# Kernel optimization log

Hardware: AMD Instinct MI355X
Metric: run time of the kernel (lower is better)

## Reference

```python
import jax, jax.numpy as jnp
import numpy as np
import math

LAMB = 0.2
N_ITERS = 3
HALF_PLUS_HALF_LOG2PI = 0.5 + 0.5 * math.log(2.0 * math.pi)  # 1/2 + log(2*pi)/2
SQRT_2PI = math.sqrt(2.0 * math.pi)


def _safe_div(num, den):
    # tf.math.divide_no_nan: 0 where denominator is 0
    den_ok = jnp.where(den == 0, 1.0, den)
    return jnp.where(den == 0, 0.0, num / den_ok)


def _m_step(act_in, R, V, bias_a, bias_b):
    # act_in: [B,ci], R: [B or 1,ci,co], V: [B,ci,co,q,s]
    odds = act_in[:, :, None] * R                                        # [B,ci,co]
    r = _safe_div(odds, jnp.sum(odds, axis=1, keepdims=True))[:, :, :, None, None]
    mu = jnp.sum(r * V, axis=1, keepdims=True)                           # [B,1,co,q,s]
    sigma = jnp.sqrt(jnp.sum(r * (V - mu) ** 2, axis=1, keepdims=True))  # [B,1,co,q,s]
    cost = jnp.sum(r * jnp.log(sigma) + HALF_PLUS_HALF_LOG2PI, axis=1)   # [B,co,q,s]
    logits = LAMB * (bias_a
                     - bias_b * jnp.sum(r, axis=(1, 3, 4))
                     - jnp.sum(cost, axis=(2, 3)))                       # [B,co]
    act_out = jax.nn.softmax(logits, axis=-1)
    return act_out, jnp.sum(mu, axis=1), sigma                           # mu -> [B,co,q,s]


def _e_step(act_out, V, mu, sigma):
    # Normal(mu, sigma).prob(V); mu broadcast over capsules_in axis
    d = V - mu[:, None]                                                  # [B,ci,co,q,s]
    prob = jnp.exp(-0.5 * d * d / (sigma * sigma)) / (sigma * SQRT_2PI)
    raw_R = act_out[:, None, :, None, None] * prob                       # [B,ci,co,q,s]
    # tf.linalg.norm(ord=1, axis=None) = global sum of |raw_R| over the whole tensor
    normed = _safe_div(raw_R, jnp.sum(jnp.abs(raw_R)))
    return jnp.sum(normed, axis=(3, 4))                                  # [B,ci,co]


def setup_inputs() -> dict:
    key = jax.random.key(0)
    k1, k2, k3, k4, k5 = jax.random.split(key, 5)
    B, CI, CO, P, S = 16, 512, 128, 8, 8
    act = jax.random.uniform(k1, (B, CI), dtype=jnp.float32)
    pose = jax.random.normal(k2, (B, CI, P, P), dtype=jnp.float32)
    transitions = 0.05 * jax.random.normal(k3, (CI, CO, P, S), dtype=jnp.float32)
    bias_a = 0.05 * jax.random.normal(k4, (CO,), dtype=jnp.float32)
    bias_b = 0.05 * jax.random.normal(k5, (CO,), dtype=jnp.float32)
    return {"act": act, "pose": pose, "transitions": transitions,
            "bias_a": bias_a, "bias_b": bias_b}


def reference(act, pose, transitions, bias_a, bias_b):
    CI = act.shape[1]
    CO = transitions.shape[1]
    posed = jnp.swapaxes(pose, -1, -2)                 # transPOSE=True
    # votes: pose[:, :, None, :, :] @ transitions  -> [B,ci,co,q,s]
    V = jnp.einsum('biqp,iops->bioqs', posed, transitions)
    R = jnp.full((1, CI, CO), 1.0 / CO, dtype=V.dtype)
    act_out, mu, sigma = _m_step(act, R, V, bias_a, bias_b)
    for _ in range(N_ITERS - 1):
        R = _e_step(act_out, V, mu, sigma)
        act_out, mu, sigma = _m_step(act, R, V, bias_a, bias_b)
    return act_out, mu
```

## Files before the change

### kernel.cpp

```cpp
#include <hip/hip_runtime.h>
#include <hip/hip_bf16.h>

#define B_    16
#define CI_   512
#define CO_   128
#define QS    64
#define NWAVE 16
#define IPW   (CI_ / NWAVE)

static constexpr float LAMB = 0.2f;
static constexpr float NEG_HALF_LOG2E = -0.72134752044448170368f;

template <int CTRL>
__device__ __forceinline__ float dpp_add(float v) {
    int x = __builtin_bit_cast(int, v);
    int y = __builtin_amdgcn_update_dpp(x, x, CTRL, 0xF, 0xF, false);
    return v + __builtin_bit_cast(float, y);
}

__device__ __forceinline__ float wave_sum64_shfl(float v) {
#pragma unroll
    for (int m = 32; m >= 1; m >>= 1) v += __shfl_xor(v, m, 64);
    return v;
}

__global__ __launch_bounds__(256) void transpose_kernel(
    const float* __restrict__ pose, const float* __restrict__ trans,
    float* __restrict__ poseT, float* __restrict__ TT)
{
    const int idx  = blockIdx.x * 256 + threadIdx.x;
    const int lane = idx & 63;
    const int row  = idx >> 6;
    const int p    = lane >> 3;
    const int c    = lane & 7;
    TT[(row << 6) + c * 8 + p] = trans[idx];
    if (idx < B_ * CI_ * QS)
        poseT[(row << 6) + c * 8 + p] = pose[idx];
}

__global__
__attribute__((amdgpu_flat_work_group_size(1024, 1024), amdgpu_waves_per_eu(4, 8)))
void capsule_kernel(
    const float* __restrict__ poseT,
    const float* __restrict__ TT,
    const float* __restrict__ act,
    const float* __restrict__ bias_a,
    const float* __restrict__ bias_b,
    float* __restrict__ logits,
    float* __restrict__ mu_out)
{
    const int blk = blockIdx.x;
    const int xcd = blk & 7;
    const int idx = blk >> 3;
    const int o   = xcd + ((idx & 15) << 3);
    const int b   = idx >> 4;

    const int tid  = threadIdx.x;
    const int wave = tid >> 6;
    const int lane = tid & 63;
    const int q    = lane >> 3;
    const int s    = lane & 7;
    const int i0   = wave * IPW;

    const float4* pT4  = (const float4*)poseT + ((size_t)(b * CI_ + i0)) * 16 + q * 2;
    const float4* tT4  = (const float4*)TT    + ((size_t)(i0 * CO_ + o)) * 16 + s * 2;
    const float*  actb = act + b * CI_ + i0;

    __shared__ __align__(16) float prbuf[NWAVE][8 * 68];
    __shared__ __align__(16) float wbuf[NWAVE * 32];
    __shared__ float sA[NWAVE][QS];
    __shared__ float sB[NWAVE][QS];
    __shared__ float sC[NWAVE];

    float* prw = prbuf[wave];

    float V[IPW];
    float Sw = 0.f, SwV = 0.f, SwV2 = 0.f;

#pragma unroll
    for (int j = 0; j < IPW; ++j) {
        float4 a0 = pT4[j * 16];
        float4 a1 = pT4[j * 16 + 1];
        float4 b0 = tT4[(size_t)j * (CO_ * 16)];
        float4 b1 = tT4[(size_t)j * (CO_ * 16) + 1];
        float v;
        v = a0.x * b0.x;
        v = fmaf(a0.y, b0.y, v);
        v = fmaf(a0.z, b0.z, v);
        v = fmaf(a0.w, b0.w, v);
        v = fmaf(a1.x, b1.x, v);
        v = fmaf(a1.y, b1.y, v);
        v = fmaf(a1.z, b1.z, v);
        v = fmaf(a1.w, b1.w, v);
        V[j] = v;
        float ai = actb[j];
        Sw  += ai;
        SwV  = fmaf(ai, v, SwV);
        SwV2 = fmaf(ai * v, v, SwV2);
    }

    auto block_reduce = [&]() {
        __syncthreads();
        sA[wave][lane] = SwV;
        sB[wave][lane] = SwV2;
        if (lane == 0) sC[wave] = Sw;
        __syncthreads();
        float a = 0.f, bb = 0.f, c = 0.f;
#pragma unroll
        for (int w = 0; w < NWAVE; ++w) {
            a  += sA[w][lane];
            bb += sB[w][lane];
            c  += sC[w];
        }
        SwV = a; SwV2 = bb; Sw = c;
    };

    block_reduce();
    float invSw = (Sw != 0.f) ? 1.f / Sw : 0.f;
    float mu  = SwV * invSw;
    float var = fmaxf(fmaf(-mu, mu, SwV2 * invSw), 1e-30f);
    float is  = 1.f / sqrtf(var);

#pragma unroll 1
    for (int it = 0; it < 2; ++it) {
        const float cc = is * is * NEG_HALF_LOG2E;
#pragma unroll
        for (int p = 0; p < 4; ++p) {
#pragma unroll
            for (int jj = 0; jj < 8; ++jj) {
                float d = V[p * 8 + jj] - mu;
                prw[jj * 68 + lane] = exp2f(d * cc * d);
            }
            const int r  = lane >> 3;
            const int co = (lane & 7) * 8;
            const float4* rp = (const float4*)&prw[r * 68 + co];
            float4 x0 = rp[0], x1 = rp[1];
            float ps = ((x0.x + x0.y) + (x0.z + x0.w)) +
                       ((x1.x + x1.y) + (x1.z + x1.w));
            ps = dpp_add<0xB1>(ps);
            ps = dpp_add<0x4E>(ps);
            ps = dpp_add<0x141>(ps);
            float wj = actb[p * 8 + r] * ps;
            if ((lane & 7) == 0) wbuf[wave * 32 + p * 8 + r] = wj;
        }
        const float4* wb4 = (const float4*)&wbuf[wave * 32];
        Sw = 0.f; SwV = 0.f; SwV2 = 0.f;
#pragma unroll
        for (int k = 0; k < 8; ++k) {
            float4 w4 = wb4[k];
            float v0 = V[4 * k + 0], v1 = V[4 * k + 1];
            float v2 = V[4 * k + 2], v3 = V[4 * k + 3];
            Sw += w4.x; SwV = fmaf(w4.x, v0, SwV); SwV2 = fmaf(w4.x * v0, v0, SwV2);
            Sw += w4.y; SwV = fmaf(w4.y, v1, SwV); SwV2 = fmaf(w4.y * v1, v1, SwV2);
            Sw += w4.z; SwV = fmaf(w4.z, v2, SwV); SwV2 = fmaf(w4.z * v2, v2, SwV2);
            Sw += w4.w; SwV = fmaf(w4.w, v3, SwV); SwV2 = fmaf(w4.w * v3, v3, SwV2);
        }
        block_reduce();
        invSw = (Sw != 0.f) ? 1.f / Sw : 0.f;
        mu  = SwV * invSw;
        var = fmaxf(fmaf(-mu, mu, SwV2 * invSw), 1e-30f);
        is  = 1.f / sqrtf(var);
    }

    if (wave == 0) {
        mu_out[((size_t)b * CO_ + o) * QS + lane] = mu;
        float sl = wave_sum64_shfl(0.5f * logf(var));
        if (lane == 0)
            logits[b * CO_ + o] = LAMB * (bias_a[o] - bias_b[o] - sl);
    }
}

__global__ __launch_bounds__(256, 4) void capsule_legacy(
    const float* __restrict__ pose,
    const float* __restrict__ trans,
    const float* __restrict__ act,
    const float* __restrict__ bias_a,
    const float* __restrict__ bias_b,
    float* __restrict__ logits,
    float* __restrict__ mu_out)
{
    const int blk  = blockIdx.x;
    const int b    = blk >> 7;
    const int o    = blk & 127;
    const int tid  = threadIdx.x;
    const int wave = tid >> 6;
    const int lane = tid & 63;
    const int q    = lane >> 3;
    const int s    = lane & 7;
    const int i0   = wave * 128;

    const float* poseb = pose + ((size_t)b * CI_ + i0) * QS + lane;
    const float* tb    = trans + ((size_t)i0 * CO_ + o) * QS + lane;
    const float* actb  = act + b * CI_ + i0;

    __shared__ float sSwV[4][QS];
    __shared__ float sSwV2[4][QS];
    __shared__ float sSw[4];

    float Sw = 0.f, SwV = 0.f, SwV2 = 0.f;

    auto do_sweep = [&](bool use_prob, float mu_r, float is_r) {
        Sw = 0.f; SwV = 0.f; SwV2 = 0.f;
        for (int j = 0; j < 128; ++j) {
            float pe = poseb[(size_t)j * QS];
            float te = tb[(size_t)j * (CO_ * QS)];
            float ai = actb[j];
            float V = 0.f;
#pragma unroll
            for (int p = 0; p < 8; ++p) {
                float a = __shfl(pe, p * 8 + q, 64);
                float t = __shfl(te, p * 8 + s, 64);
                V = fmaf(a, t, V);
            }
            float w;
            if (use_prob) {
                float d  = V - mu_r;
                float e  = d * is_r;
                float pr = is_r * exp2f(e * e * NEG_HALF_LOG2E);
                w = ai * wave_sum64_shfl(pr);
            } else {
                w = ai;
            }
            Sw += w;
            SwV  = fmaf(w, V, SwV);
            SwV2 = fmaf(w * V, V, SwV2);
        }
        __syncthreads();
        sSwV[wave][lane]  = SwV;
        sSwV2[wave][lane] = SwV2;
        if (lane == 0) sSw[wave] = Sw;
        __syncthreads();
        float a = 0.f, c = 0.f, d2 = 0.f;
#pragma unroll
        for (int w2 = 0; w2 < 4; ++w2) {
            a  += sSwV[w2][lane];
            d2 += sSwV2[w2][lane];
            c  += sSw[w2];
        }
        SwV = a; SwV2 = d2; Sw = c;
    };

    float mu = 0.f, var = 1.f, is = 1.f;
    do_sweep(false, 0.f, 0.f);
    {
        float invSw = (Sw != 0.f) ? 1.f / Sw : 0.f;
        mu = SwV * invSw; var = fmaxf(fmaf(-mu, mu, SwV2 * invSw), 1e-30f);
        is = 1.f / sqrtf(var);
    }
    do_sweep(true, mu, is);
    {
        float invSw = (Sw != 0.f) ? 1.f / Sw : 0.f;
        mu = SwV * invSw; var = fmaxf(fmaf(-mu, mu, SwV2 * invSw), 1e-30f);
        is = 1.f / sqrtf(var);
    }
    do_sweep(true, mu, is);
    {
        float invSw = (Sw != 0.f) ? 1.f / Sw : 0.f;
        mu = SwV * invSw; var = fmaxf(fmaf(-mu, mu, SwV2 * invSw), 1e-30f);
    }

    if (wave == 0) {
        mu_out[((size_t)b * CO_ + o) * QS + lane] = mu;
        float sl = wave_sum64_shfl(0.5f * logf(var));
        if (lane == 0)
            logits[b * CO_ + o] = LAMB * (bias_a[o] - bias_b[o] - sl);
    }
}

__global__ __launch_bounds__(128) void softmax_kernel(
    const float* __restrict__ logits, float* __restrict__ out)
{
    const int b = blockIdx.x;
    const int t = threadIdx.x;
    float l = logits[b * CO_ + t];

    __shared__ float sm[2];
    __shared__ float s2[2];

    float m = l;
#pragma unroll
    for (int k = 32; k >= 1; k >>= 1) m = fmaxf(m, __shfl_xor(m, k, 64));
    if ((t & 63) == 0) sm[t >> 6] = m;
    __syncthreads();
    m = fmaxf(sm[0], sm[1]);

    float e = expf(l - m);
    float ssum = e;
#pragma unroll
    for (int k = 32; k >= 1; k >>= 1) ssum += __shfl_xor(ssum, k, 64);
    if ((t & 63) == 0) s2[t >> 6] = ssum;
    __syncthreads();
    float tot = s2[0] + s2[1];

    out[b * CO_ + t] = e / tot;
}

extern "C" void kernel_launch(void* const* d_in, const int* in_sizes, int n_in,
                              void* d_out, int out_size, void* d_ws, size_t ws_size,
                              hipStream_t stream) {
    const float *act = nullptr, *pose = nullptr, *trans = nullptr;
    const float *bias_a = nullptr, *bias_b = nullptr;
    for (int i = 0; i < n_in; ++i) {
        const float* p = (const float*)d_in[i];
        switch (in_sizes[i]) {
            case 8192:    act = p; break;
            case 524288:  pose = p; break;
            case 4194304: trans = p; break;
            case 128:     if (!bias_a) bias_a = p; else bias_b = p; break;
            default: break;
        }
    }
    if (!act || !pose || !trans || !bias_a || !bias_b) {
        act    = (const float*)d_in[0];
        pose   = (const float*)d_in[1];
        trans  = (const float*)d_in[2];
        bias_a = (const float*)d_in[3];
        bias_b = (const float*)d_in[4];
    }

    float* out_act = (float*)d_out;
    float* out_mu  = out_act + B_ * CO_;

    const size_t NEEDED = (size_t)(524288 + 4194304 + 2048) * 4;

    if (ws_size >= NEEDED) {
        float* poseT  = (float*)d_ws;
        float* TT     = poseT + 524288;
        float* logits = TT + 4194304;

        transpose_kernel<<<dim3(4194304 / 256), dim3(256), 0, stream>>>(
            pose, trans, poseT, TT);
        capsule_kernel<<<dim3(B_ * CO_), dim3(1024), 0, stream>>>(
            poseT, TT, act, bias_a, bias_b, logits, out_mu);
        softmax_kernel<<<dim3(B_), dim3(128), 0, stream>>>(logits, out_act);
    } else {
        float* logits = (float*)d_ws;
        capsule_legacy<<<dim3(B_ * CO_), dim3(256), 0, stream>>>(
            pose, trans, act, bias_a, bias_b, logits, out_mu);
        softmax_kernel<<<dim3(B_), dim3(128), 0, stream>>>(logits, out_act);
    }
}
```

Baseline: 277.4 us.

## Process eight batches per block to reuse transition slices across batches

Each block now loops over eight batch entries for a single output capsule, shrinking the grid from 2048 to 256 blocks and remapping blocks to XCDs by capsule. The intent is to reuse the same transition matrix data from cache across batches and cut launch/scheduling overhead. In exchange, each block does serialized work with fewer concurrent blocks per CU, reducing latency hiding across the many barriers.

```diff
diff --git a/kernel.cpp b/kernel.cpp
--- a/kernel.cpp
+++ b/kernel.cpp
@@ -49,11 +49,11 @@
     float* __restrict__ logits,
     float* __restrict__ mu_out)
 {
-    const int blk = blockIdx.x;
-    const int xcd = blk & 7;
-    const int idx = blk >> 3;
-    const int o   = xcd + ((idx & 15) << 3);
-    const int b   = idx >> 4;
+    const int bi = blockIdx.x;
+    const int x  = bi & 7;
+    const int y  = bi >> 3;
+    const int o  = x * 16 + (y & 15);
+    const int b0 = (y >> 4) * 8;
 
     const int tid  = threadIdx.x;
     const int wave = tid >> 6;
@@ -62,9 +62,7 @@
     const int s    = lane & 7;
     const int i0   = wave * IPW;
 
-    const float4* pT4  = (const float4*)poseT + ((size_t)(b * CI_ + i0)) * 16 + q * 2;
-    const float4* tT4  = (const float4*)TT    + ((size_t)(i0 * CO_ + o)) * 16 + s * 2;
-    const float*  actb = act + b * CI_ + i0;
+    const float4* tT4 = (const float4*)TT + (i0 * CO_ + o) * 16 + s * 2;
 
     __shared__ __align__(16) float prbuf[NWAVE][8 * 68];
     __shared__ __align__(16) float wbuf[NWAVE * 32];
@@ -74,99 +72,105 @@
 
     float* prw = prbuf[wave];
 
-    float V[IPW];
-    float Sw = 0.f, SwV = 0.f, SwV2 = 0.f;
-
-#pragma unroll
-    for (int j = 0; j < IPW; ++j) {
-        float4 a0 = pT4[j * 16];
-        float4 a1 = pT4[j * 16 + 1];
-        float4 b0 = tT4[(size_t)j * (CO_ * 16)];
-        float4 b1 = tT4[(size_t)j * (CO_ * 16) + 1];
-        float v;
-        v = a0.x * b0.x;
-        v = fmaf(a0.y, b0.y, v);
-        v = fmaf(a0.z, b0.z, v);
-        v = fmaf(a0.w, b0.w, v);
-        v = fmaf(a1.x, b1.x, v);
-        v = fmaf(a1.y, b1.y, v);
-        v = fmaf(a1.z, b1.z, v);
-        v = fmaf(a1.w, b1.w, v);
-        V[j] = v;
-        float ai = actb[j];
-        Sw  += ai;
-        SwV  = fmaf(ai, v, SwV);
-        SwV2 = fmaf(ai * v, v, SwV2);
-    }
-
-    auto block_reduce = [&]() {
-        __syncthreads();
-        sA[wave][lane] = SwV;
-        sB[wave][lane] = SwV2;
-        if (lane == 0) sC[wave] = Sw;
-        __syncthreads();
-        float a = 0.f, bb = 0.f, c = 0.f;
-#pragma unroll
-        for (int w = 0; w < NWAVE; ++w) {
-            a  += sA[w][lane];
-            bb += sB[w][lane];
-            c  += sC[w];
-        }
-        SwV = a; SwV2 = bb; Sw = c;
-    };
-
-    block_reduce();
-    float invSw = (Sw != 0.f) ? 1.f / Sw : 0.f;
-    float mu  = SwV * invSw;
-    float var = fmaxf(fmaf(-mu, mu, SwV2 * invSw), 1e-30f);
-    float is  = 1.f / sqrtf(var);
+    for (int pair = 0; pair < 8; ++pair) {
+        const int b = b0 + pair;
+        const float4* pT4  = (const float4*)poseT + (b * CI_ + i0) * 16 + q * 2;
+        const float*  actb = act + b * CI_ + i0;
+
+        float V[IPW];
+        float Sw = 0.f, SwV = 0.f, SwV2 = 0.f;
+
+#pragma unroll
+        for (int j = 0; j < IPW; ++j) {
+            float4 a0 = pT4[j * 16];
+            float4 a1 = pT4[j * 16 + 1];
+            float4 b0v = tT4[j * (CO_ * 16)];
+            float4 b1v = tT4[j * (CO_ * 16) + 1];
+            float v;
+            v = a0.x * b0v.x;
+            v = fmaf(a0.y, b0v.y, v);
+            v = fmaf(a0.z, b0v.z, v);
+            v = fmaf(a0.w, b0v.w, v);
+            v = fmaf(a1.x, b1v.x, v);
+            v = fmaf(a1.y, b1v.y, v);
+            v = fmaf(a1.z, b1v.z, v);
+            v = fmaf(a1.w, b1v.w, v);
+            V[j] = v;
+            float ai = actb[j];
+            Sw  += ai;
+            SwV  = fmaf(ai, v, SwV);
+            SwV2 = fmaf(ai * v, v, SwV2);
+        }
+
+        auto block_reduce = [&]() {
+            __syncthreads();
+            sA[wave][lane] = SwV;
+            sB[wave][lane] = SwV2;
+            if (lane == 0) sC[wave] = Sw;
+            __syncthreads();
+            float a = 0.f, bb = 0.f, c = 0.f;
+#pragma unroll
+            for (int w = 0; w < NWAVE; ++w) {
+                a  += sA[w][lane];
+                bb += sB[w][lane];
+                c  += sC[w];
+            }
+            SwV = a; SwV2 = bb; Sw = c;
+        };
+
+        block_reduce();
+        float invSw = (Sw != 0.f) ? 1.f / Sw : 0.f;
+        float mu  = SwV * invSw;
+        float var = fmaxf(fmaf(-mu, mu, SwV2 * invSw), 1e-30f);
+        float is  = 1.f / sqrtf(var);
 
 #pragma unroll 1
-    for (int it = 0; it < 2; ++it) {
-        const float cc = is * is * NEG_HALF_LOG2E;
-#pragma unroll
-        for (int p = 0; p < 4; ++p) {
-#pragma unroll
-            for (int jj = 0; jj < 8; ++jj) {
-                float d = V[p * 8 + jj] - mu;
-                prw[jj * 68 + lane] = exp2f(d * cc * d);
-            }
-            const int r  = lane >> 3;
-            const int co = (lane & 7) * 8;
-            const float4* rp = (const float4*)&prw[r * 68 + co];
-            float4 x0 = rp[0], x1 = rp[1];
-            float ps = ((x0.x + x0.y) + (x0.z + x0.w)) +
-                       ((x1.x + x1.y) + (x1.z + x1.w));
-            ps = dpp_add<0xB1>(ps);
-            ps = dpp_add<0x4E>(ps);
-            ps = dpp_add<0x141>(ps);
-            float wj = actb[p * 8 + r] * ps;
-            if ((lane & 7) == 0) wbuf[wave * 32 + p * 8 + r] = wj;
-        }
-        const float4* wb4 = (const float4*)&wbuf[wave * 32];
-        Sw = 0.f; SwV = 0.f; SwV2 = 0.f;
-#pragma unroll
-        for (int k = 0; k < 8; ++k) {
-            float4 w4 = wb4[k];
-            float v0 = V[4 * k + 0], v1 = V[4 * k + 1];
-            float v2 = V[4 * k + 2], v3 = V[4 * k + 3];
-            Sw += w4.x; SwV = fmaf(w4.x, v0, SwV); SwV2 = fmaf(w4.x * v0, v0, SwV2);
-            Sw += w4.y; SwV = fmaf(w4.y, v1, SwV); SwV2 = fmaf(w4.y * v1, v1, SwV2);
-            Sw += w4.z; SwV = fmaf(w4.z, v2, SwV); SwV2 = fmaf(w4.z * v2, v2, SwV2);
-            Sw += w4.w; SwV = fmaf(w4.w, v3, SwV); SwV2 = fmaf(w4.w * v3, v3, SwV2);
-        }
-        block_reduce();
-        invSw = (Sw != 0.f) ? 1.f / Sw : 0.f;
-        mu  = SwV * invSw;
-        var = fmaxf(fmaf(-mu, mu, SwV2 * invSw), 1e-30f);
-        is  = 1.f / sqrtf(var);
-    }
-
-    if (wave == 0) {
-        mu_out[((size_t)b * CO_ + o) * QS + lane] = mu;
-        float sl = wave_sum64_shfl(0.5f * logf(var));
-        if (lane == 0)
-            logits[b * CO_ + o] = LAMB * (bias_a[o] - bias_b[o] - sl);
+        for (int it = 0; it < 2; ++it) {
+            const float cc = is * is * NEG_HALF_LOG2E;
+#pragma unroll
+            for (int p = 0; p < 4; ++p) {
+#pragma unroll
+                for (int jj = 0; jj < 8; ++jj) {
+                    float d = V[p * 8 + jj] - mu;
+                    prw[jj * 68 + lane] = exp2f(d * cc * d);
+                }
+                const int r  = lane >> 3;
+                const int co = (lane & 7) * 8;
+                const float4* rp = (const float4*)&prw[r * 68 + co];
+                float4 x0 = rp[0], x1 = rp[1];
+                float ps = ((x0.x + x0.y) + (x0.z + x0.w)) +
+                           ((x1.x + x1.y) + (x1.z + x1.w));
+                ps = dpp_add<0xB1>(ps);
+                ps = dpp_add<0x4E>(ps);
+                ps = dpp_add<0x141>(ps);
+                float wj = actb[p * 8 + r] * ps;
+                if ((lane & 7) == 0) wbuf[wave * 32 + p * 8 + r] = wj;
+            }
+            const float4* wb4 = (const float4*)&wbuf[wave * 32];
+            Sw = 0.f; SwV = 0.f; SwV2 = 0.f;
+#pragma unroll
+            for (int k = 0; k < 8; ++k) {
+                float4 w4 = wb4[k];
+                float v0 = V[4 * k + 0], v1 = V[4 * k + 1];
+                float v2 = V[4 * k + 2], v3 = V[4 * k + 3];
+                Sw += w4.x; SwV = fmaf(w4.x, v0, SwV); SwV2 = fmaf(w4.x * v0, v0, SwV2);
+                Sw += w4.y; SwV = fmaf(w4.y, v1, SwV); SwV2 = fmaf(w4.y * v1, v1, SwV2);
+                Sw += w4.z; SwV = fmaf(w4.z, v2, SwV); SwV2 = fmaf(w4.z * v2, v2, SwV2);
+                Sw += w4.w; SwV = fmaf(w4.w, v3, SwV); SwV2 = fmaf(w4.w * v3, v3, SwV2);
+            }
+            block_reduce();
+            invSw = (Sw != 0.f) ? 1.f / Sw : 0.f;
+            mu  = SwV * invSw;
+            var = fmaxf(fmaf(-mu, mu, SwV2 * invSw), 1e-30f);
+            is  = 1.f / sqrtf(var);
+        }
+
+        if (wave == 0) {
+            mu_out[(b * CO_ + o) * QS + lane] = mu;
+            float sl = wave_sum64_shfl(0.5f * logf(var));
+            if (lane == 0)
+                logits[b * CO_ + o] = LAMB * (bias_a[o] - bias_b[o] - sl);
+        }
     }
 }
 
@@ -330,7 +334,7 @@
 
         transpose_kernel<<<dim3(4194304 / 256), dim3(256), 0, stream>>>(
             pose, trans, poseT, TT);
-        capsule_kernel<<<dim3(B_ * CO_), dim3(1024), 0, stream>>>(
+        capsule_kernel<<<dim3(256), dim3(1024), 0, stream>>>(
             poseT, TT, act, bias_a, bias_b, logits, out_mu);
         softmax_kernel<<<dim3(B_), dim3(128), 0, stream>>>(logits, out_act);
     } else {
```

Result: slower. 626.9 us (+126.0%).
